# Optimization experiments

Hardware: AMD Instinct MI355X
Metric: run time of the kernel (lower is better)

The kernel has to match this reference:

```python
import jax, jax.numpy as jnp
import numpy as np

CROP = 7  # feature_genetic1 crop size
NCH = 1024  # channels looped over in feature_genetic1


def _genetic(x, ih, iw):
    # x: [B, 1024, H, W]; ih, iw: [1024] per-channel random crop offsets in [0,7)
    ch = jnp.arange(NCH)
    rows = ih[:, None] + jnp.arange(CROP)          # [1024, 7]
    cols = iw[:, None] + jnp.arange(CROP)          # [1024, 7]
    # fused gather: out[b, c, i, j] = x[b, c, ih[c]+i, iw[c]+j]
    return x[:, ch[:, None, None], rows[:, :, None], cols[:, None, :]]  # [B,1024,7,7]


def _avg_pool_5s2p2(x):
    # torch F.avg_pool2d(x, 5, stride=2, padding=2), count_include_pad=True
    s = jax.lax.reduce_window(x, 0.0, jax.lax.add,
                              (1, 1, 5, 5), (1, 1, 2, 2),
                              ((0, 0), (0, 0), (2, 2), (2, 2)))
    return s / 25.0


def setup_inputs() -> dict:
    key = jax.random.key(0)
    ks = jax.random.split(key, 10)
    B = 64
    return {
        "x1": jax.random.normal(ks[0], (B, 1024, 14, 14), jnp.float32),
        "x2": jax.random.normal(ks[1], (B, 1024, 14, 14), jnp.float32),
        "x3": jax.random.normal(ks[2], (B, 1280, 28, 28), jnp.float32),
        "share_feature": jax.random.normal(ks[3], (B, 1024, 14, 14), jnp.float32),
        "c_w": jax.random.normal(ks[4], (1024, 1280), jnp.float32) * 0.02,
        "conv3d_w": jax.random.normal(ks[5], (32, 16, 3, 3, 3), jnp.float32) * 0.05,
        "lin_w": jax.random.normal(ks[6], (768, 1), jnp.float32) * 0.02,
        "lin_b": jax.random.normal(ks[7], (1,), jnp.float32),
        "idx_h": jax.random.randint(ks[8], (4, 1024), 0, 7, jnp.int32),
        "idx_w": jax.random.randint(ks[9], (4, 1024), 0, 7, jnp.int32),
    }


def reference(x1, x2, x3, share_feature, c_w, conv3d_w, lin_w, lin_b, idx_h, idx_w):
    B = x1.shape[0]
    # x3 path: avg_pool2d(5, 2, 2) -> Conv2d(1280->1024, 1x1, no bias)
    x3p = _avg_pool_5s2p2(x3)                                  # [B,1280,14,14]
    x3p = jnp.einsum('bchw,oc->bohw', x3p, c_w)                # [B,1024,14,14]
    # four per-channel random-crop gathers (the 1024-iter python loop, fused)
    g1 = _genetic(x1, idx_h[0], idx_w[0])
    g2 = _genetic(x2, idx_h[1], idx_w[1])
    g3 = _genetic(x3p, idx_h[2], idx_w[2])
    gs = _genetic(share_feature, idx_h[3], idx_w[3])
    xa = jnp.concatenate([g1, g2], axis=2)                     # [B,1024,14,7]
    xb = jnp.concatenate([g3, gs], axis=2)                     # [B,1024,14,7]
    x = jnp.concatenate([xa, xb], axis=3)                      # [B,1024,14,14]
    x = x.reshape(B, 16, 64, 14, 14)
    # Conv3d(16->32, k=3, stride=(3,1,1), pad=(4,1,1), no bias): depth 64 -> 24
    x = jax.lax.conv_general_dilated(
        x, conv3d_w, window_strides=(3, 1, 1),
        padding=((4, 4), (1, 1), (1, 1)),
        dimension_numbers=('NCDHW', 'OIDHW', 'NCDHW'))         # [B,32,24,14,14]
    x = x.reshape(B, 768, 14, 14)
    # ViT stub: global average pool; head: Linear(768 -> 1)
    x = x.mean(axis=(2, 3))                                    # [B,768]
    return x @ lin_w + lin_b                                   # [B,1]
```

## Files before the change

kernel.cpp:

```cpp
#include <hip/hip_runtime.h>

#define NCH 1024

typedef float f4v __attribute__((ext_vector_type(4)));


__global__ void k2_maps(const float* __restrict__ w3,
                        const float* __restrict__ lin_w,
                        const int* __restrict__ idx_h,
                        const int* __restrict__ idx_w,
                        float* __restrict__ A1,
                        float* __restrict__ A2,
                        float* __restrict__ As,
                        float* __restrict__ G3) {
  __shared__ float lweff[9];
  int c = blockIdx.x;
  int t = threadIdx.x;
  int dd = c & 63, ich = c >> 6;
  int kd = (dd + 4) % 3;
  int d  = (dd + 4 - kd) / 3;
  if (t < 9) {
    float acc = 0.f;
    for (int o = 0; o < 32; ++o)
      acc += lin_w[o * 24 + d] * w3[(((o * 16 + ich) * 3) + kd) * 9 + t];
    lweff[t] = acc * (1.f / 196.f);
  }
  __syncthreads();
  if (t >= 196) return;
  float weff[9];
#pragma unroll
  for (int k = 0; k < 9; ++k) weff[k] = lweff[k];
  float rh[3][3];
#pragma unroll
  for (int kw = 0; kw < 3; ++kw) {
    rh[0][kw] = weff[0 * 3 + kw] + weff[1 * 3 + kw];
    rh[1][kw] = weff[0 * 3 + kw] + weff[1 * 3 + kw] + weff[2 * 3 + kw];
    rh[2][kw] = weff[1 * 3 + kw] + weff[2 * 3 + kw];
  }
  float p[9];
#pragma unroll
  for (int hc = 0; hc < 3; ++hc) {
    p[hc * 3 + 0] = rh[hc][0] + rh[hc][1];
    p[hc * 3 + 1] = rh[hc][0] + rh[hc][1] + rh[hc][2];
    p[hc * 3 + 2] = rh[hc][1] + rh[hc][2];
  }
  int h = t / 14, w = t % 14;
  {
    int i = h - idx_h[0 * NCH + c], j = w - idx_w[0 * NCH + c];
    bool in = (i >= 0 && i < 7 && j >= 0 && j < 7);
    int hc = (i == 0) ? 0 : 1, wc = (j == 0) ? 0 : 1;
    A1[c * 196 + t] = in ? p[hc * 3 + wc] : 0.f;
  }
  {
    int i = h - idx_h[1 * NCH + c], j = w - idx_w[1 * NCH + c];
    bool in = (i >= 0 && i < 7 && j >= 0 && j < 7);
    int hc = (i == 6) ? 2 : 1, wc = (j == 0) ? 0 : 1;
    A2[c * 196 + t] = in ? p[hc * 3 + wc] : 0.f;
  }
  {
    int i = h - idx_h[3 * NCH + c], j = w - idx_w[3 * NCH + c];
    bool in = (i >= 0 && i < 7 && j >= 0 && j < 7);
    int hc = (i == 6) ? 2 : 1, wc = (j == 6) ? 2 : 1;
    As[c * 196 + t] = in ? p[hc * 3 + wc] : 0.f;
  }
  {
    int i = h - idx_h[2 * NCH + c], j = w - idx_w[2 * NCH + c];
    bool in = (i >= 0 && i < 7 && j >= 0 && j < 7);
    int hc = (i == 0) ? 0 : 1, wc = (j == 6) ? 2 : 1;
    G3[c * 196 + t] = in ? p[hc * 3 + wc] : 0.f;
  }
}

__global__ __launch_bounds__(256) void k3_vgemm(const float* __restrict__ c_w,
                                                const float* __restrict__ G3,
                                                float* __restrict__ Vp) {
  __shared__ float cwT[64][64];
  __shared__ float g3t[64][64];
  int cc0 = blockIdx.x * 64;
  int p0 = blockIdx.y * 64;
  int kz = blockIdx.z;
  int tid = threadIdx.x;
  int lane = tid & 63, wid = tid >> 6;
  int tc = lane & 15;
  int pq = wid * 4 + (lane >> 4);
  float acc[4][4];
#pragma unroll
  for (int i = 0; i < 4; ++i)
#pragma unroll
    for (int j = 0; j < 4; ++j) acc[i][j] = 0.f;
  for (int k0 = kz * 128; k0 < kz * 128 + 128; k0 += 64) {
#pragma unroll
    for (int r = 0; r < 4; ++r) {
      int idx4 = r * 256 + tid;
      int kk = idx4 >> 4, c4 = idx4 & 15;
      *(float4*)&cwT[kk][c4 * 4] =
          *(const float4*)&c_w[(size_t)(k0 + kk) * 1280 + cc0 + c4 * 4];
    }
#pragma unroll
    for (int r = 0; r < 4; ++r) {
      int idx4 = r * 256 + tid;
      int kk = idx4 >> 4, p4 = idx4 & 15;
      int p = p0 + p4 * 4;
      float4 v = (p < 196) ? *(const float4*)&G3[(size_t)(k0 + kk) * 196 + p]
                           : float4{0.f, 0.f, 0.f, 0.f};
      *(float4*)&g3t[kk][p4 * 4] = v;
    }
    __syncthreads();
#pragma unroll
    for (int kk = 0; kk < 64; ++kk) {
      float4 a = *(const float4*)&cwT[kk][tc * 4];
      float4 b = *(const float4*)&g3t[kk][pq * 4];
      acc[0][0] += a.x * b.x; acc[0][1] += a.x * b.y; acc[0][2] += a.x * b.z; acc[0][3] += a.x * b.w;
      acc[1][0] += a.y * b.x; acc[1][1] += a.y * b.y; acc[1][2] += a.y * b.z; acc[1][3] += a.y * b.w;
      acc[2][0] += a.z * b.x; acc[2][1] += a.z * b.y; acc[2][2] += a.z * b.z; acc[2][3] += a.z * b.w;
      acc[3][0] += a.w * b.x; acc[3][1] += a.w * b.y; acc[3][2] += a.w * b.z; acc[3][3] += a.w * b.w;
    }
    __syncthreads();
  }
  int p = p0 + pq * 4;
  if (p < 196) {
#pragma unroll
    for (int i = 0; i < 4; ++i) {
      int cc = cc0 + tc * 4 + i;
      *(float4*)&Vp[(size_t)kz * 250880 + (size_t)cc * 196 + p] =
          float4{acc[i][0], acc[i][1], acc[i][2], acc[i][3]};
    }
  }
}

__global__ void k4_unpool(const float* __restrict__ Vp, float* __restrict__ U) {
  __shared__ float v[196];
  int cc = blockIdx.x;
  int t = threadIdx.x;
  if (t < 196) {
    float s = 0.f;
#pragma unroll
    for (int z = 0; z < 8; ++z)
      s += Vp[(size_t)z * 250880 + (size_t)cc * 196 + t];
    v[t] = s;
  }
  __syncthreads();
  for (int q = t; q < 784; q += blockDim.x) {
    int H = q / 28, W = q % 28;
    int hlo = (H - 1) / 2; if (hlo < 0) hlo = 0;
    int hhi = (H + 2) / 2; if (hhi > 13) hhi = 13;
    int wlo = (W - 1) / 2; if (wlo < 0) wlo = 0;
    int whi = (W + 2) / 2; if (whi > 13) whi = 13;
    float s = 0.f;
    for (int h = hlo; h <= hhi; ++h)
      for (int w = wlo; w <= whi; ++w) s += v[h * 14 + w];
    U[(size_t)cc * 784 + q] = s * 0.04f;
  }
}

__global__ __launch_bounds__(256) void kdot(const f4v* __restrict__ x1,
                                            const f4v* __restrict__ x2,
                                            const f4v* __restrict__ xs,
                                            const f4v* __restrict__ x3,
                                            const f4v* __restrict__ A,
                                            const f4v* __restrict__ U,
                                            float* __restrict__ part) {
  int bid = blockIdx.x;
  int z, bg, cx;
  size_t stride;
  const f4v *xbase, *wbase;
  if (bid < 588) {
    z = bid / 196;
    int rr = bid % 196;
    cx = rr >> 2;
    bg = rr & 3;
    const f4v* xt = (z == 0) ? x1 : (z == 1) ? x2 : xs;
    stride = 50176;
    xbase = xt + (size_t)bg * 16 * 50176 + (size_t)cx * 1024;
    wbase = A + (size_t)z * 50176 + (size_t)cx * 1024;
  } else {
    int rr = bid - 588;
    z = 3;
    cx = rr >> 2;
    bg = rr & 3;
    stride = 250880;
    xbase = x3 + (size_t)bg * 16 * 250880 + (size_t)cx * 1024;
    wbase = U + (size_t)cx * 1024;
  }
  int t = threadIdx.x;
  float s[16];
#pragma unroll
  for (int i = 0; i < 16; ++i) s[i] = 0.f;
#pragma unroll
  for (int u = 0; u < 4; ++u) {
    f4v w = wbase[u * 256 + t];
#pragma unroll
    for (int b = 0; b < 16; ++b) {
      f4v a =
          __builtin_nontemporal_load(&xbase[(size_t)b * stride + u * 256 + t]);
      s[b] += a.x * w.x + a.y * w.y + a.z * w.z + a.w * w.w;
    }
  }
  int lane = t & 63, wid = t >> 6;
  __shared__ float red[16][4];
#pragma unroll
  for (int b = 0; b < 16; ++b) {
    float v = s[b];
#pragma unroll
    for (int off = 32; off > 0; off >>= 1) v += __shfl_down(v, off, 64);
    if (lane == 0) red[b][wid] = v;
  }
  __syncthreads();
  if (t < 16) {
    float r4 = red[t][0] + red[t][1] + red[t][2] + red[t][3];
    int row = z * 64 + bg * 16 + t;
    part[(row << 8) + cx] = r4;
  }
}

__global__ void k7_final(const float* __restrict__ part,
                         const float* __restrict__ lin_b,
                         float* __restrict__ out) {
  int b = threadIdx.x;
  if (b >= 64) return;
  float s = lin_b[0];
  for (int z = 0; z < 3; ++z)
#pragma unroll
    for (int cx = 0; cx < 49; ++cx) s += part[((z * 64 + b) << 8) + cx];
#pragma unroll
  for (int cx = 0; cx < 245; ++cx) s += part[((192 + b) << 8) + cx];
  out[b] = s;
}

extern "C" void kernel_launch(void* const* d_in, const int* in_sizes, int n_in,
                              void* d_out, int out_size, void* d_ws, size_t ws_size,
                              hipStream_t stream) {
  const float* x1 = (const float*)d_in[0];
  const float* x2 = (const float*)d_in[1];
  const float* x3 = (const float*)d_in[2];
  const float* sf = (const float*)d_in[3];
  const float* c_w = (const float*)d_in[4];
  const float* w3 = (const float*)d_in[5];
  const float* lin_w = (const float*)d_in[6];
  const float* lin_b = (const float*)d_in[7];
  const int* idx_h = (const int*)d_in[8];
  const int* idx_w = (const int*)d_in[9];
  float* out = (float*)d_out;
  float* ws = (float*)d_ws;

  float* A = ws;
  float* G3 = A + 602112;
  float* Vp = G3 + 200704;
  float* U = Vp + 2007040;
  float* part = U + 1003520;

  k2_maps<<<dim3(1024), dim3(256), 0, stream>>>(w3, lin_w, idx_h, idx_w,
                                                A, A + 200704, A + 2 * 200704, G3);
  k3_vgemm<<<dim3(20, 4, 8), dim3(256), 0, stream>>>(c_w, G3, Vp);
  k4_unpool<<<dim3(1280), dim3(256), 0, stream>>>(Vp, U);
  kdot<<<dim3(1568), dim3(256), 0, stream>>>(
      (const f4v*)x1, (const f4v*)x2, (const f4v*)sf,
      (const f4v*)x3, (const f4v*)A, (const f4v*)U, part);
  k7_final<<<dim3(1), dim3(64), 0, stream>>>(part, lin_b, out);
}
```

Before: 140.5 us.

## Restructure kdot to one wave per batch row with weights staged in LDS

Measured after the change: 142.7 us. About the same (+1.5%).

```diff
diff --git a/kernel.cpp b/kernel.cpp
--- a/kernel.cpp
+++ b/kernel.cpp
@@ -153,64 +153,52 @@
   }
 }
 
-__global__ __launch_bounds__(256) void kdot(const f4v* __restrict__ x1,
+__global__ __launch_bounds__(512) void kdot(const f4v* __restrict__ x1,
                                             const f4v* __restrict__ x2,
                                             const f4v* __restrict__ xs,
                                             const f4v* __restrict__ x3,
                                             const f4v* __restrict__ A,
                                             const f4v* __restrict__ U,
                                             float* __restrict__ part) {
+  __shared__ f4v lw[1024];
   int bid = blockIdx.x;
   int z, bg, cx;
   size_t stride;
-  const f4v *xbase, *wbase;
-  if (bid < 588) {
-    z = bid / 196;
-    int rr = bid % 196;
-    cx = rr >> 2;
-    bg = rr & 3;
-    const f4v* xt = (z == 0) ? x1 : (z == 1) ? x2 : xs;
+  const f4v *xt, *wbase;
+  if (bid < 1176) {
+    z = bid / 392;
+    int rr = bid % 392;
+    cx = rr >> 3;
+    bg = rr & 7;
+    xt = (z == 0) ? x1 : (z == 1) ? x2 : xs;
     stride = 50176;
-    xbase = xt + (size_t)bg * 16 * 50176 + (size_t)cx * 1024;
     wbase = A + (size_t)z * 50176 + (size_t)cx * 1024;
   } else {
-    int rr = bid - 588;
+    int rr = bid - 1176;
     z = 3;
-    cx = rr >> 2;
-    bg = rr & 3;
+    cx = rr >> 3;
+    bg = rr & 7;
+    xt = x3;
     stride = 250880;
-    xbase = x3 + (size_t)bg * 16 * 250880 + (size_t)cx * 1024;
     wbase = U + (size_t)cx * 1024;
   }
   int t = threadIdx.x;
-  float s[16];
-#pragma unroll
-  for (int i = 0; i < 16; ++i) s[i] = 0.f;
-#pragma unroll
-  for (int u = 0; u < 4; ++u) {
-    f4v w = wbase[u * 256 + t];
-#pragma unroll
-    for (int b = 0; b < 16; ++b) {
-      f4v a =
-          __builtin_nontemporal_load(&xbase[(size_t)b * stride + u * 256 + t]);
-      s[b] += a.x * w.x + a.y * w.y + a.z * w.z + a.w * w.w;
-    }
-  }
-  int lane = t & 63, wid = t >> 6;
-  __shared__ float red[16][4];
-#pragma unroll
-  for (int b = 0; b < 16; ++b) {
-    float v = s[b];
-#pragma unroll
-    for (int off = 32; off > 0; off >>= 1) v += __shfl_down(v, off, 64);
-    if (lane == 0) red[b][wid] = v;
-  }
+  lw[t] = wbase[t];
+  lw[512 + t] = wbase[512 + t];
   __syncthreads();
-  if (t < 16) {
-    float r4 = red[t][0] + red[t][1] + red[t][2] + red[t][3];
-    int row = z * 64 + bg * 16 + t;
-    part[(row << 8) + cx] = r4;
-  }
+  int w = t >> 6, lane = t & 63;
+  int b = bg * 8 + w;
+  const f4v* xb = xt + (size_t)b * stride + (size_t)cx * 1024;
+  float s = 0.f;
+#pragma unroll
+  for (int i = 0; i < 16; ++i) {
+    f4v a = xb[i * 64 + lane];
+    f4v ww = lw[i * 64 + lane];
+    s += a.x * ww.x + a.y * ww.y + a.z * ww.z + a.w * ww.w;
+  }
+#pragma unroll
+  for (int off = 32; off > 0; off >>= 1) s += __shfl_down(s, off, 64);
+  if (lane == 0) part[((z * 64 + b) << 8) + cx] = s;
 }
 
 __global__ void k7_final(const float* __restrict__ part,
@@ -253,7 +241,7 @@
                                                 A, A + 200704, A + 2 * 200704, G3);
   k3_vgemm<<<dim3(20, 4, 8), dim3(256), 0, stream>>>(c_w, G3, Vp);
   k4_unpool<<<dim3(1280), dim3(256), 0, stream>>>(Vp, U);
-  kdot<<<dim3(1568), dim3(256), 0, stream>>>(
+  kdot<<<dim3(3136), dim3(512), 0, stream>>>(
       (const f4v*)x1, (const f4v*)x2, (const f4v*)sf,
       (const f4v*)x3, (const f4v*)A, (const f4v*)U, part);
   k7_final<<<dim3(1), dim3(64), 0, stream>>>(part, lin_b, out);
```
